# Performance work log

Measured on AMD Instinct MI355X. Metric: run time of the kernel, lower is better.

Reference implementation:

```python
import jax, jax.numpy as jnp
import numpy as np

EPS = 1e-5

def exp_map_zero(v):
    # Poincare ball exp map at origin: tanh(||v||) * v / ||v||
    norm = jnp.clip(jnp.linalg.norm(v, axis=-1, keepdims=True), EPS, None)
    return jnp.tanh(jnp.clip(norm, None, 15.0)) * v / norm

def poincare_pairwise_distance(x, c):
    # x: [N, D] points in the ball, c: [K, D] points in the ball -> [N, K]
    x2 = jnp.sum(x * x, axis=-1)                      # [N]
    c2 = jnp.sum(c * c, axis=-1)                      # [K]
    sqdiff = x2[:, None] + c2[None, :] - 2.0 * (x @ c.T)   # ||x-c||^2, [N, K]
    sqdiff = jnp.clip(sqdiff, 0.0, None)
    denom = jnp.clip((1.0 - x2)[:, None] * (1.0 - c2)[None, :], EPS, None)
    arg = jnp.clip(1.0 + 2.0 * sqdiff / denom, 1.0 + 1e-7, None)
    return jnp.arccosh(arg)

def setup_inputs() -> dict:
    key = jax.random.key(0)
    k1, k2, k3 = jax.random.split(key, 3)
    N, K, D = 200000, 128, 128
    node_repr = jax.random.normal(k1, (N, D), dtype=jnp.float32) * 0.05  # inside unit ball
    mask = jnp.ones((N, 1), dtype=jnp.float32)
    centroid_weight = jax.random.normal(k2, (K, D), dtype=jnp.float32) * 0.05
    return {"node_repr": node_repr, "mask": mask, "centroid_weight": centroid_weight}

def reference(node_repr, mask, centroid_weight):
    # euclidean embed_manifold path: map centroid params onto the ball first
    centroid_repr = exp_map_zero(centroid_weight)                  # [K, D]
    dist = poincare_pairwise_distance(node_repr, centroid_repr)    # [N, K]
    node_centroid_dist = dist[None, :, :] * mask                   # [1, N, K] (mask [N,1] broadcasts)
    graph_centroid_dist = jnp.sum(node_centroid_dist, axis=1) / jnp.sum(mask)  # [1, K]
    return (graph_centroid_dist, node_centroid_dist)
```

## Files before the change

### kernel.cpp

```cpp
#include <hip/hip_runtime.h>
#include <hip/hip_bf16.h>
#include <math.h>

#define EPSF 1e-5f

constexpr int D = 128;
constexpr int K = 128;
constexpr int TILE_ROWS = 64;
constexpr int BPITCH = 272;
constexpr int NBG = 1024;

typedef __bf16 bf16x8 __attribute__((ext_vector_type(8)));
typedef float  f32x4  __attribute__((ext_vector_type(4)));

__global__ __launch_bounds__(64) void prep_kernel(const float* __restrict__ w,
                                                  __bf16* __restrict__ crb,
                                                  float* __restrict__ c2) {
    int k = blockIdx.x;
    int t = threadIdx.x;
    float a = w[k * D + t];
    float b = w[k * D + t + 64];
    float ss = a * a + b * b;
#pragma unroll
    for (int off = 1; off < 64; off <<= 1)
        ss += __shfl_xor(ss, off, 64);
    float nrm   = sqrtf(ss);
    float nclip = fmaxf(nrm, EPSF);
    float targ  = fminf(nclip, 15.0f);
    float th    = tanhf(targ);
    float s     = th / nclip;
    crb[k * D + t]      = (__bf16)(a * s);
    crb[k * D + t + 64] = (__bf16)(b * s);
    if (t == 0) {
        float cn = s * nrm;
        c2[k] = cn * cn;
    }
}

__global__ __launch_bounds__(256) void main_kernel(
        const float* __restrict__ x, const float* __restrict__ mask,
        const __bf16* __restrict__ crb, const float* __restrict__ c2g,
        float* __restrict__ out_node, float* __restrict__ partial,
        float* __restrict__ maskpart, int ntiles) {
    __shared__ __align__(16) unsigned char sB[K * BPITCH];
    __shared__ float sC2[K];
    __shared__ float sCol[4][K];
    __shared__ float sM[4];

    const int t    = threadIdx.x;
    const int wave = t >> 6;
    const int lane = t & 63;
    const int m    = lane & 15;
    const int q    = lane >> 4;
    const int bid  = blockIdx.x;
    const int stride = gridDim.x;

#pragma unroll
    for (int i = 0; i < 8; i++) {
        int f4  = t + 256 * i;
        int row = f4 >> 4;
        int c4  = f4 & 15;
        float4 v = ((const float4*)crb)[f4];
        *(float4*)(sB + row * BPITCH + c4 * 16) = v;
    }
    if (t < K) sC2[t] = c2g[t];

    float colsum[8] = {0.f, 0.f, 0.f, 0.f, 0.f, 0.f, 0.f, 0.f};
    float msumacc = 0.f;

    __syncthreads();

    for (int tile = bid; tile < ntiles; tile += stride) {
        const float* xrow = x + (size_t)(tile * TILE_ROWS + wave * 16 + m) * D + q * 8;
        float4 xr[8];
#pragma unroll
        for (int s = 0; s < 4; s++) {
            xr[2 * s]     = *(const float4*)(xrow + s * 32);
            xr[2 * s + 1] = *(const float4*)(xrow + s * 32 + 4);
        }
        float mk = mask[tile * TILE_ROWS + wave * 16 + m];

        float ssq = 0.f;
        bf16x8 av[4];
#pragma unroll
        for (int s = 0; s < 4; s++) {
            float4 a0 = xr[2 * s], a1 = xr[2 * s + 1];
            ssq += a0.x*a0.x + a0.y*a0.y + a0.z*a0.z + a0.w*a0.w
                 + a1.x*a1.x + a1.y*a1.y + a1.z*a1.z + a1.w*a1.w;
            av[s][0] = (__bf16)a0.x; av[s][1] = (__bf16)a0.y;
            av[s][2] = (__bf16)a0.z; av[s][3] = (__bf16)a0.w;
            av[s][4] = (__bf16)a1.x; av[s][5] = (__bf16)a1.y;
            av[s][6] = (__bf16)a1.z; av[s][7] = (__bf16)a1.w;
        }
        ssq += __shfl_xor(ssq, 16, 64);
        ssq += __shfl_xor(ssq, 32, 64);
        float mred = mk;
        mred += __shfl_xor(mred, 1, 64);
        mred += __shfl_xor(mred, 2, 64);
        mred += __shfl_xor(mred, 4, 64);
        mred += __shfl_xor(mred, 8, 64);
        msumacc += mred;
        float x2r[4], pxr[4], mvr[4];
#pragma unroll
        for (int i = 0; i < 4; i++) {
            x2r[i] = __shfl(ssq, q * 4 + i, 64);
            pxr[i] = 1.0f - x2r[i];
            mvr[i] = __shfl(mk, q * 4 + i, 64);
        }

        f32x4 acc[8] = {};
#pragma unroll
        for (int s = 0; s < 4; s++) {
#pragma unroll
            for (int tk = 0; tk < 8; tk++) {
                bf16x8 bv = *(const bf16x8*)(sB + (tk * 16 + m) * BPITCH + q * 16 + s * 64);
                acc[tk] = __builtin_amdgcn_mfma_f32_16x16x32_bf16(av[s], bv, acc[tk], 0, 0, 0);
            }
        }

        float dv[8][4];
#pragma unroll
        for (int tk = 0; tk < 8; tk++) {
            float c2c = sC2[tk * 16 + m];
            float pc  = 1.0f - c2c;
#pragma unroll
            for (int i = 0; i < 4; i++) {
                float dot = acc[tk][i];
                float sq  = fmaxf(x2r[i] + c2c - 2.0f * dot, 0.0f);
                float den = fmaxf(pxr[i] * pc, EPSF);
                float arg = fmaf(2.0f * sq, __builtin_amdgcn_rcpf(den), 1.0f);
                arg = fmaxf(arg, 1.0f + 1e-7f);
                float dist = __logf(arg + __builtin_amdgcn_sqrtf(fmaf(arg, arg, -1.0f)));
                float val = dist * mvr[i];
                dv[tk][i] = val;
                colsum[tk] += val;
            }
        }

        const int rowq = tile * TILE_ROWS + wave * 16 + q * 4;
        float* obase = out_node + (size_t)rowq * K + m;
#pragma unroll
        for (int tk = 0; tk < 8; tk++) {
#pragma unroll
            for (int i = 0; i < 4; i++)
                __builtin_nontemporal_store(dv[tk][i], obase + (size_t)i * K + tk * 16);
        }
    }

#pragma unroll
    for (int tk = 0; tk < 8; tk++) {
        colsum[tk] += __shfl_xor(colsum[tk], 16, 64);
        colsum[tk] += __shfl_xor(colsum[tk], 32, 64);
    }
    if (lane < 16) {
#pragma unroll
        for (int tk = 0; tk < 8; tk++)
            sCol[wave][tk * 16 + lane] = colsum[tk];
    }
    if (lane == 0) sM[wave] = msumacc;

    __syncthreads();

    if (t < K)
        partial[(size_t)bid * K + t] =
            sCol[0][t] + sCol[1][t] + sCol[2][t] + sCol[3][t];
    if (t == 0)
        maskpart[bid] = sM[0] + sM[1] + sM[2] + sM[3];
}

__global__ __launch_bounds__(256) void reduce_kernel(
        const float* __restrict__ partial, const float* __restrict__ maskpart,
        float* __restrict__ out_graph, int NB) {
    int k = blockIdx.x;
    int t = threadIdx.x;
    float s = 0.f, mm = 0.f;
    for (int b = t; b < NB; b += 256) {
        s  += partial[(size_t)b * K + k];
        mm += maskpart[b];
    }
#pragma unroll
    for (int off = 1; off < 64; off <<= 1) {
        s  += __shfl_xor(s, off, 64);
        mm += __shfl_xor(mm, off, 64);
    }
    __shared__ float rs[4], rm[4];
    int w = t >> 6;
    if ((t & 63) == 0) { rs[w] = s; rm[w] = mm; }
    __syncthreads();
    if (t == 0) {
        float st = rs[0] + rs[1] + rs[2] + rs[3];
        float mt = rm[0] + rm[1] + rm[2] + rm[3];
        out_graph[k] = st / mt;
    }
}

extern "C" void kernel_launch(void* const* d_in, const int* in_sizes, int n_in,
                              void* d_out, int out_size, void* d_ws, size_t ws_size,
                              hipStream_t stream) {
    const float* node = (const float*)d_in[0];
    const float* mask = (const float*)d_in[1];
    const float* w    = (const float*)d_in[2];
    float* out = (float*)d_out;

    int N      = in_sizes[0] / D;
    int ntiles = N / TILE_ROWS;
    int nbg    = NBG < ntiles ? NBG : ntiles;

    __bf16* crb     = (__bf16*)d_ws;
    float* c2       = (float*)(crb + K * D);
    float* partial  = c2 + K;
    float* maskpart = partial + (size_t)nbg * K;

    float* out_graph = out;
    float* out_node  = out + K;

    prep_kernel<<<K, 64, 0, stream>>>(w, crb, c2);
    main_kernel<<<nbg, 256, 0, stream>>>(node, mask, crb, c2, out_node,
                                         partial, maskpart, ntiles);
    reduce_kernel<<<K, 256, 0, stream>>>(partial, maskpart, out_graph, nbg);
}
```

Before: 206.4 us.

## Launch one block per tile and read centroids from global/L2 instead of LDS

Replaces the persistent grid-stride kernel (1024 blocks looping over tiles with centroids staged in shared memory) with one block per 64-row tile, 3125 blocks in total. Each block reads the bf16 centroid matrix and c2 straight from global memory, relying on L1/L2 caching, and uses nontemporal loads for x and mask. This removes the LDS staging and its barrier and raises occupancy, since shared memory use drops sharply. The cost is many more redundant centroid reads through cache and a partial buffer that is three times larger for the reduce kernel to sum.

After: 235.0 us. +13.9%, slower.

```diff
diff --git a/kernel.cpp b/kernel.cpp
--- a/kernel.cpp
+++ b/kernel.cpp
@@ -7,8 +7,6 @@
 constexpr int D = 128;
 constexpr int K = 128;
 constexpr int TILE_ROWS = 64;
-constexpr int BPITCH = 272;
-constexpr int NBG = 1024;
 
 typedef __bf16 bf16x8 __attribute__((ext_vector_type(8)));
 typedef float  f32x4  __attribute__((ext_vector_type(4)));
@@ -42,8 +40,6 @@
         const __bf16* __restrict__ crb, const float* __restrict__ c2g,
         float* __restrict__ out_node, float* __restrict__ partial,
         float* __restrict__ maskpart, int ntiles) {
-    __shared__ __align__(16) unsigned char sB[K * BPITCH];
-    __shared__ float sC2[K];
     __shared__ float sCol[4][K];
     __shared__ float sM[4];
 
@@ -52,99 +48,91 @@
     const int lane = t & 63;
     const int m    = lane & 15;
     const int q    = lane >> 4;
-    const int bid  = blockIdx.x;
-    const int stride = gridDim.x;
-
-#pragma unroll
-    for (int i = 0; i < 8; i++) {
-        int f4  = t + 256 * i;
-        int row = f4 >> 4;
-        int c4  = f4 & 15;
-        float4 v = ((const float4*)crb)[f4];
-        *(float4*)(sB + row * BPITCH + c4 * 16) = v;
-    }
-    if (t < K) sC2[t] = c2g[t];
-
-    float colsum[8] = {0.f, 0.f, 0.f, 0.f, 0.f, 0.f, 0.f, 0.f};
-    float msumacc = 0.f;
-
-    __syncthreads();
-
-    for (int tile = bid; tile < ntiles; tile += stride) {
-        const float* xrow = x + (size_t)(tile * TILE_ROWS + wave * 16 + m) * D + q * 8;
-        float4 xr[8];
-#pragma unroll
-        for (int s = 0; s < 4; s++) {
-            xr[2 * s]     = *(const float4*)(xrow + s * 32);
-            xr[2 * s + 1] = *(const float4*)(xrow + s * 32 + 4);
-        }
-        float mk = mask[tile * TILE_ROWS + wave * 16 + m];
-
-        float ssq = 0.f;
-        bf16x8 av[4];
-#pragma unroll
-        for (int s = 0; s < 4; s++) {
-            float4 a0 = xr[2 * s], a1 = xr[2 * s + 1];
-            ssq += a0.x*a0.x + a0.y*a0.y + a0.z*a0.z + a0.w*a0.w
-                 + a1.x*a1.x + a1.y*a1.y + a1.z*a1.z + a1.w*a1.w;
-            av[s][0] = (__bf16)a0.x; av[s][1] = (__bf16)a0.y;
-            av[s][2] = (__bf16)a0.z; av[s][3] = (__bf16)a0.w;
-            av[s][4] = (__bf16)a1.x; av[s][5] = (__bf16)a1.y;
-            av[s][6] = (__bf16)a1.z; av[s][7] = (__bf16)a1.w;
-        }
-        ssq += __shfl_xor(ssq, 16, 64);
-        ssq += __shfl_xor(ssq, 32, 64);
-        float mred = mk;
-        mred += __shfl_xor(mred, 1, 64);
-        mred += __shfl_xor(mred, 2, 64);
-        mred += __shfl_xor(mred, 4, 64);
-        mred += __shfl_xor(mred, 8, 64);
-        msumacc += mred;
-        float x2r[4], pxr[4], mvr[4];
+    const int rowbase = blockIdx.x * TILE_ROWS + wave * 16;
+
+    float c2v[8];
+#pragma unroll
+    for (int tk = 0; tk < 8; tk++) c2v[tk] = c2g[tk * 16 + m];
+
+    const float* xrow = x + (size_t)(rowbase + m) * D + q * 8;
+    float ssq = 0.f;
+    bf16x8 av[4];
+#pragma unroll
+    for (int h = 0; h < 2; h++) {
+        f32x4 xr[4];
+#pragma unroll
+        for (int s2 = 0; s2 < 2; s2++) {
+            int s = h * 2 + s2;
+            xr[2 * s2]     = __builtin_nontemporal_load((const f32x4*)(xrow + s * 32));
+            xr[2 * s2 + 1] = __builtin_nontemporal_load((const f32x4*)(xrow + s * 32 + 4));
+        }
+#pragma unroll
+        for (int s2 = 0; s2 < 2; s2++) {
+            int s = h * 2 + s2;
+            f32x4 a0 = xr[2 * s2], a1 = xr[2 * s2 + 1];
+            ssq += a0[0]*a0[0] + a0[1]*a0[1] + a0[2]*a0[2] + a0[3]*a0[3]
+                 + a1[0]*a1[0] + a1[1]*a1[1] + a1[2]*a1[2] + a1[3]*a1[3];
+            av[s][0] = (__bf16)a0[0]; av[s][1] = (__bf16)a0[1];
+            av[s][2] = (__bf16)a0[2]; av[s][3] = (__bf16)a0[3];
+            av[s][4] = (__bf16)a1[0]; av[s][5] = (__bf16)a1[1];
+            av[s][6] = (__bf16)a1[2]; av[s][7] = (__bf16)a1[3];
+        }
+    }
+    float mk = __builtin_nontemporal_load(mask + rowbase + m);
+
+    ssq += __shfl_xor(ssq, 16, 64);
+    ssq += __shfl_xor(ssq, 32, 64);
+    float mred = mk;
+    mred += __shfl_xor(mred, 1, 64);
+    mred += __shfl_xor(mred, 2, 64);
+    mred += __shfl_xor(mred, 4, 64);
+    mred += __shfl_xor(mred, 8, 64);
+    float x2r[4], pxr[4], mvr[4];
+#pragma unroll
+    for (int i = 0; i < 4; i++) {
+        x2r[i] = __shfl(ssq, q * 4 + i, 64);
+        pxr[i] = 1.0f - x2r[i];
+        mvr[i] = __shfl(mk, q * 4 + i, 64);
+    }
+
+    f32x4 acc[8] = {};
+#pragma unroll
+    for (int s = 0; s < 4; s++) {
+#pragma unroll
+        for (int tk = 0; tk < 8; tk++) {
+            bf16x8 bv = *(const bf16x8*)(crb + (size_t)(tk * 16 + m) * D + q * 8 + s * 32);
+            acc[tk] = __builtin_amdgcn_mfma_f32_16x16x32_bf16(av[s], bv, acc[tk], 0, 0, 0);
+        }
+        __builtin_amdgcn_sched_barrier(0);
+    }
+
+    float colsum[8];
+#pragma unroll
+    for (int tk = 0; tk < 8; tk++) {
+        float c2c = c2v[tk];
+        float pc  = 1.0f - c2c;
+        colsum[tk] = 0.f;
 #pragma unroll
         for (int i = 0; i < 4; i++) {
-            x2r[i] = __shfl(ssq, q * 4 + i, 64);
-            pxr[i] = 1.0f - x2r[i];
-            mvr[i] = __shfl(mk, q * 4 + i, 64);
-        }
-
-        f32x4 acc[8] = {};
-#pragma unroll
-        for (int s = 0; s < 4; s++) {
-#pragma unroll
-            for (int tk = 0; tk < 8; tk++) {
-                bf16x8 bv = *(const bf16x8*)(sB + (tk * 16 + m) * BPITCH + q * 16 + s * 64);
-                acc[tk] = __builtin_amdgcn_mfma_f32_16x16x32_bf16(av[s], bv, acc[tk], 0, 0, 0);
-            }
-        }
-
-        float dv[8][4];
-#pragma unroll
-        for (int tk = 0; tk < 8; tk++) {
-            float c2c = sC2[tk * 16 + m];
-            float pc  = 1.0f - c2c;
-#pragma unroll
-            for (int i = 0; i < 4; i++) {
-                float dot = acc[tk][i];
-                float sq  = fmaxf(x2r[i] + c2c - 2.0f * dot, 0.0f);
-                float den = fmaxf(pxr[i] * pc, EPSF);
-                float arg = fmaf(2.0f * sq, __builtin_amdgcn_rcpf(den), 1.0f);
-                arg = fmaxf(arg, 1.0f + 1e-7f);
-                float dist = __logf(arg + __builtin_amdgcn_sqrtf(fmaf(arg, arg, -1.0f)));
-                float val = dist * mvr[i];
-                dv[tk][i] = val;
-                colsum[tk] += val;
-            }
-        }
-
-        const int rowq = tile * TILE_ROWS + wave * 16 + q * 4;
-        float* obase = out_node + (size_t)rowq * K + m;
-#pragma unroll
-        for (int tk = 0; tk < 8; tk++) {
-#pragma unroll
-            for (int i = 0; i < 4; i++)
-                __builtin_nontemporal_store(dv[tk][i], obase + (size_t)i * K + tk * 16);
-        }
+            float dot = acc[tk][i];
+            float sq  = fmaxf(x2r[i] + c2c - 2.0f * dot, 0.0f);
+            float den = fmaxf(pxr[i] * pc, EPSF);
+            float arg = fmaf(2.0f * sq, __builtin_amdgcn_rcpf(den), 1.0f);
+            arg = fmaxf(arg, 1.0f + 1e-7f);
+            float dist = __logf(arg + __builtin_amdgcn_sqrtf(fmaf(arg, arg, -1.0f)));
+            float val = dist * mvr[i];
+            acc[tk][i] = val;
+            colsum[tk] += val;
+        }
+    }
+
+    const int rowq = rowbase + q * 4;
+    float* obase = out_node + (size_t)rowq * K + m;
+#pragma unroll
+    for (int tk = 0; tk < 8; tk++) {
+#pragma unroll
+        for (int i = 0; i < 4; i++)
+            __builtin_nontemporal_store(acc[tk][i], obase + (size_t)i * K + tk * 16);
     }
 
 #pragma unroll
@@ -157,15 +145,15 @@
         for (int tk = 0; tk < 8; tk++)
             sCol[wave][tk * 16 + lane] = colsum[tk];
     }
-    if (lane == 0) sM[wave] = msumacc;
+    if (lane == 0) sM[wave] = mred;
 
     __syncthreads();
 
     if (t < K)
-        partial[(size_t)bid * K + t] =
+        partial[(size_t)blockIdx.x * K + t] =
             sCol[0][t] + sCol[1][t] + sCol[2][t] + sCol[3][t];
     if (t == 0)
-        maskpart[bid] = sM[0] + sM[1] + sM[2] + sM[3];
+        maskpart[blockIdx.x] = sM[0] + sM[1] + sM[2] + sM[3];
 }
 
 __global__ __launch_bounds__(256) void reduce_kernel(
@@ -202,20 +190,19 @@
     const float* w    = (const float*)d_in[2];
     float* out = (float*)d_out;
 
-    int N      = in_sizes[0] / D;
-    int ntiles = N / TILE_ROWS;
-    int nbg    = NBG < ntiles ? NBG : ntiles;
+    int N  = in_sizes[0] / D;
+    int NB = N / TILE_ROWS;
 
     __bf16* crb     = (__bf16*)d_ws;
     float* c2       = (float*)(crb + K * D);
     float* partial  = c2 + K;
-    float* maskpart = partial + (size_t)nbg * K;
+    float* maskpart = partial + (size_t)NB * K;
 
     float* out_graph = out;
     float* out_node  = out + K;
 
     prep_kernel<<<K, 64, 0, stream>>>(w, crb, c2);
-    main_kernel<<<nbg, 256, 0, stream>>>(node, mask, crb, c2, out_node,
-                                         partial, maskpart, ntiles);
-    reduce_kernel<<<K, 256, 0, stream>>>(partial, maskpart, out_graph, nbg);
-}
+    main_kernel<<<NB, 256, 0, stream>>>(node, mask, crb, c2, out_node,
+                                        partial, maskpart, NB);
+    reduce_kernel<<<K, 256, 0, stream>>>(partial, maskpart, out_graph, NB);
+}
```
